# Performance work log

Measured on AMD Instinct MI355X. Metric: run time of the kernel, lower is better.

Reference implementation:

```python
import jax, jax.numpy as jnp
import numpy as np

B, T, INP, E, H, N = 16, 256, 1536, 512, 8, 16
D = E // H            # 64, must equal default dim_head for to_out shapes to work
SCALE = D ** -0.5
EPS = 1e-5


def _ln(x, g, b):
    m = x.mean(-1, keepdims=True)
    v = ((x - m) ** 2).mean(-1, keepdims=True)
    return (x - m) * jax.lax.rsqrt(v + EPS) * g + b


def _attend(q, k, v, Wo, bo):
    # q,k,v: [bt, h, n, d]. NOTE: attend is LogSoftmax, not Softmax (faithful).
    dots = jnp.einsum('bhnd,bhmd->bhnm', q, k) * SCALE
    a = jax.nn.log_softmax(dots, axis=-1)
    o = jnp.einsum('bhnm,bhmd->bhnd', a, v)
    o = o.transpose(0, 2, 1, 3).reshape(o.shape[0], N, E)  # b n (h d)
    return o @ Wo + bo


def _self_attn(x, Wqkv, Wo, bo):
    # x is already LayerNormed (PreNorm); residual adds the normed x (faithful).
    qkv = x @ Wqkv  # [bt, n, 3E]
    q, k, v = jnp.split(qkv, 3, axis=-1)
    hd = lambda t: t.reshape(t.shape[0], N, H, D).transpose(0, 2, 1, 3)
    return _attend(hd(q), hd(k), hd(v), Wo, bo) + x


def _ff(x, W1, b1, W2, b2):
    # x already LayerNormed; residual adds normed x (faithful to PreNorm+FF).
    return jax.nn.gelu(x @ W1 + b1, approximate=False) @ W2 + b2 + x


def setup_inputs() -> dict:
    key = jax.random.key(0)
    ks = iter(jax.random.split(key, 64))
    nrm = lambda shape, s=0.02: jax.random.normal(next(ks), shape, jnp.float32) * s
    inp = {
        'features': jax.random.normal(next(ks), (B, T, INP), jnp.float32),
        'targets_array': jax.random.randint(next(ks), (B, T), 0, N, jnp.int64),
        'emb': nrm((N, E), 1.0),
        'Wf': nrm((INP, 2 * E * N)), 'bf': jnp.zeros((2 * E * N,), jnp.float32),
        # layer 0: Attention (tuple path: only to_out used)
        'att0_Wo': nrm((E, E)), 'att0_bo': jnp.zeros((E,), jnp.float32),
        'Wm': nrm((E, 1)), 'bm': jnp.zeros((1,), jnp.float32),
    }
    for i in range(3):
        inp[f'ff{i}_g'] = jnp.ones((E,), jnp.float32)
        inp[f'ff{i}_b'] = jnp.zeros((E,), jnp.float32)
        inp[f'ff{i}_W1'] = nrm((E, 2 * E)); inp[f'ff{i}_b1'] = jnp.zeros((2 * E,), jnp.float32)
        inp[f'ff{i}_W2'] = nrm((2 * E, E)); inp[f'ff{i}_b2'] = jnp.zeros((E,), jnp.float32)
    for i in (1, 2):
        inp[f'att{i}_g'] = jnp.ones((E,), jnp.float32)
        inp[f'att{i}_b'] = jnp.zeros((E,), jnp.float32)
        inp[f'att{i}_Wqkv'] = nrm((E, 3 * E))
        inp[f'att{i}_Wo'] = nrm((E, E)); inp[f'att{i}_bo'] = jnp.zeros((E,), jnp.float32)
    return inp


def reference(features, targets_array, emb, Wf, bf, att0_Wo, att0_bo, Wm, bm,
              ff0_g, ff0_b, ff0_W1, ff0_b1, ff0_W2, ff0_b2,
              ff1_g, ff1_b, ff1_W1, ff1_b1, ff1_W2, ff1_b2,
              ff2_g, ff2_b, ff2_W1, ff2_b1, ff2_W2, ff2_b2,
              att1_g, att1_b, att1_Wqkv, att1_Wo, att1_bo,
              att2_g, att2_b, att2_Wqkv, att2_Wo, att2_bo):
    f = features.reshape(-1, INP)                 # [BT, INP]
    t = targets_array.reshape(-1)                 # [BT]
    kv = f @ Wf + bf                              # [BT, 2*E*N]
    k_, v_ = jnp.split(kv, 2, axis=-1)
    nhd = lambda x: x.reshape(-1, N, H, D).transpose(0, 2, 1, 3)  # b (n h d) -> b h n d
    k, v = nhd(k_), nhd(v_)
    q = emb[t].reshape(-1, H, 1, D)               # b h d -> b h 1 d
    q = jnp.broadcast_to(q, (q.shape[0], H, N, D))
    # layer stack: Attn(tuple), PreNorm(FF), PreNorm(Attn), PreNorm(FF), PreNorm(Attn), PreNorm(FF)
    x = _attend(q, k, v, att0_Wo, att0_bo)        # [BT, N, E]
    x = _ff(_ln(x, ff0_g, ff0_b), ff0_W1, ff0_b1, ff0_W2, ff0_b2)
    x = _self_attn(_ln(x, att1_g, att1_b), att1_Wqkv, att1_Wo, att1_bo)
    x = _ff(_ln(x, ff1_g, ff1_b), ff1_W1, ff1_b1, ff1_W2, ff1_b2)
    x = _self_attn(_ln(x, att2_g, att2_b), att2_Wqkv, att2_Wo, att2_bo)
    x = _ff(_ln(x, ff2_g, ff2_b), ff2_W1, ff2_b1, ff2_W2, ff2_b2)
    out = x.mean(axis=1)                          # mean over targets -> [BT, E]
    out = out.reshape(B, T, E)
    mean = out @ Wm + bm                          # [B, T, 1]
    return mean
```

## Files before the change

kernel.cpp:

```cpp
#include <hip/hip_runtime.h>
#include <math.h>

#define BTOT 4096
#define INP  1536
#define EDIM 512
#define NTOK 16
#define KVW  16384
#define ENW  8192
#define FFH  1024
#define NDOT 2048

typedef __attribute__((ext_vector_type(8))) __bf16 bf16x8;
typedef __attribute__((ext_vector_type(4))) float f32x4;

__device__ __forceinline__ ushort f2bf(float f) {
    union { float f; unsigned u; } v; v.f = f;
    unsigned r = v.u + 0x7fffu + ((v.u >> 16) & 1u);
    return (ushort)(r >> 16);
}
__device__ __forceinline__ float bf2f(ushort h) {
    union { unsigned u; float f; } v; v.u = ((unsigned)h) << 16;
    return v.f;
}

struct TJob { const float* in; ushort* out; int ld, c0, R, gbx, boffs; };

struct PrepArgs {
    const float* features; ushort* featb;
    const float* wq0; const float* wq1; ushort* wv0; ushort* wv1;
    const float* Wf; const float* bfv; const float* emb;
    ushort* BTg; float* C0s; const int* targets; int* perm; int* boff;
    TJob tj[10];
};

__global__ __launch_bounds__(256) void prep_all_k(PrepArgs A)
{
    __shared__ float t[64][65];
    __shared__ int cnt[NTOK], off_s[NTOK], cur[NTOK];
    const int b = blockIdx.x;
    const int tid = threadIdx.x;

    if (b < 3328) {
        if (b < 3072) {
            const int i = b * 256 + tid;
            const float4* p = reinterpret_cast<const float4*>(A.features) + 2 * (size_t)i;
            float4 a = p[0], c = p[1];
            uint4 o;
            o.x = f2bf(a.x) | ((unsigned)f2bf(a.y) << 16);
            o.y = f2bf(a.z) | ((unsigned)f2bf(a.w) << 16);
            o.z = f2bf(c.x) | ((unsigned)f2bf(c.y) << 16);
            o.w = f2bf(c.z) | ((unsigned)f2bf(c.w) << 16);
            reinterpret_cast<uint4*>(A.featb)[i] = o;
        } else {
            const int bb = b - 3072;
            const float* src = (bb >= 128) ? A.wq1 : A.wq0;
            ushort* dst = (bb >= 128) ? A.wv1 : A.wv0;
            const int idx = (bb & 127) * 256 + tid;
            const int row = idx >> 6, c8 = (idx & 63) * 8;
            const float4* p = reinterpret_cast<const float4*>(
                src + (size_t)row * (3 * EDIM) + 2 * EDIM + c8);
            float4 a = p[0], c = p[1];
            uint4 o;
            o.x = f2bf(a.x) | ((unsigned)f2bf(a.y) << 16);
            o.y = f2bf(a.z) | ((unsigned)f2bf(a.w) << 16);
            o.z = f2bf(c.x) | ((unsigned)f2bf(c.y) << 16);
            o.w = f2bf(c.z) | ((unsigned)f2bf(c.w) << 16);
            *reinterpret_cast<uint4*>(dst + (size_t)row * EDIM + c8) = o;
        }
        return;
    }

    if (b < 4480) {
        const int gb = b - 3328;
        const int hm = gb & 127;
        const int gby = gb >> 7;
        if (gby == 8) {
            if (hm != 0) return;
            if (tid < NTOK) cnt[tid] = 0;
            __syncthreads();
            for (int i = tid; i < BTOT; i += 256) atomicAdd(&cnt[A.targets[i]], 1);
            __syncthreads();
            if (tid == 0) {
                int s = 0;
                for (int bk = 0; bk < NTOK; ++bk) { off_s[bk] = s; cur[bk] = s; s += cnt[bk]; }
                for (int bk = 0; bk < NTOK; ++bk) A.boff[bk] = off_s[bk];
                A.boff[NTOK] = s;
            }
            __syncthreads();
            for (int i = tid; i < BTOT; i += 256) {
                int tt = A.targets[i];
                int p = atomicAdd(&cur[tt], 1);
                A.perm[p] = i;
            }
            return;
        }
        const int h = hm >> 4, m = hm & 15;
        const int l = tid & 63, w = tid >> 6;
        const int tk = l & 15, isub = l >> 4;
        const int colb = m * 512 + h * 64;
        const int ibase = gby * (INP / 8);

        float4 e[16];
#pragma unroll
        for (int q = 0; q < 16; ++q)
            e[q] = *reinterpret_cast<const float4*>(A.emb + tk * EDIM + h * 64 + q * 4);

        const int n = tk * 128 + hm;
        for (int i0 = ibase; i0 < ibase + INP / 8; i0 += 16) {
            const int i = i0 + w * 4 + isub;
            const float* wr = A.Wf + (size_t)i * KVW + colb;
            float acc = 0.f;
#pragma unroll
            for (int q = 0; q < 16; ++q) {
                float4 v4 = *reinterpret_cast<const float4*>(wr + q * 4);
                acc = fmaf(v4.x, e[q].x, fmaf(v4.y, e[q].y,
                      fmaf(v4.z, e[q].z, fmaf(v4.w, e[q].w, acc))));
            }
            A.BTg[(size_t)n * INP + i] = f2bf(acc);
        }
        if (gby == 0 && w == 0 && isub == 0) {
            const float* br = A.bfv + colb;
            float acc = 0.f;
#pragma unroll
            for (int q = 0; q < 16; ++q) {
                float4 v4 = *reinterpret_cast<const float4*>(br + q * 4);
                acc = fmaf(v4.x, e[q].x, fmaf(v4.y, e[q].y,
                      fmaf(v4.z, e[q].z, fmaf(v4.w, e[q].w, acc))));
            }
            A.C0s[n] = 0.125f * acc;
        }
        return;
    }

    const int rel = b - 4480;
    int ji = 0;
    while (ji < 9 && rel >= A.tj[ji + 1].boffs) ++ji;
    TJob jb = A.tj[ji];
    const int r2 = rel - jb.boffs;
    const int bx = r2 % jb.gbx, by = r2 / jb.gbx;

    const int bc = bx * 64 + jb.c0;
    const int br = by * 64;
#pragma unroll
    for (int it = 0; it < 16; ++it) {
        int idx = tid + it * 256;
        int r = idx >> 6, c = idx & 63;
        t[r][c] = jb.in[(size_t)(br + r) * jb.ld + bc + c];
    }
    __syncthreads();
    const int C0 = bx * 64;
#pragma unroll
    for (int it = 0; it < 4; ++it) {
        int idx = tid + it * 256;
        int cc = idx >> 4, rp = idx & 15;
        uint2 w2;
        w2.x = f2bf(t[4 * rp + 0][cc]) | ((unsigned)f2bf(t[4 * rp + 1][cc]) << 16);
        w2.y = f2bf(t[4 * rp + 2][cc]) | ((unsigned)f2bf(t[4 * rp + 3][cc]) << 16);
        *reinterpret_cast<uint2*>(jb.out + (size_t)(C0 + cc) * jb.R + br + 4 * rp) = w2;
    }
}

template <int BM, int BN, int WM, int WN, int NW, bool GELU, bool OUTBF>
__global__ __launch_bounds__(NW * 64) void gemm_mfma_k(
    const ushort* __restrict__ A, int lda,
    const ushort* __restrict__ BT, int ldb,
    void* __restrict__ Cp, int ldc, int K,
    const float* __restrict__ bias,
    const float* __restrict__ res, int ldr,
    float scale)
{
    static_assert((BM / WM) * (BN / WN) == NW, "wave grid");
    static_assert(BM % (NW * 8) == 0 && BN % (NW * 8) == 0, "staging");
    constexpr int FM = WM / 16, FN = WN / 16;
    constexpr int IA = BM * 8 / (NW * 64), IB = BN * 8 / (NW * 64);
    constexpr int RA = BM / NW, RB = BN / NW;

    __shared__ bf16x8 As[BM][8];
    __shared__ bf16x8 Bs[BN][8];
    const int tid = threadIdx.x;
    const int l   = tid & 63;
    const int w   = tid >> 6;
    const int wm  = w / (BN / WN), wn = w % (BN / WN);
    const int brow = blockIdx.y * BM, bcol = blockIdx.x * BN;

    const int lr = l >> 3;
    const int ls = (l & 7) ^ lr;
    const ushort* Ab = A  + (size_t)(brow + w * RA + lr) * lda + ls * 8;
    const ushort* Bb = BT + (size_t)(bcol + w * RB + lr) * ldb + ls * 8;

    f32x4 acc[FM][FN];
#pragma unroll
    for (int i = 0; i < FM; ++i)
#pragma unroll
        for (int j = 0; j < FN; ++j) acc[i][j] = (f32x4)0.f;

    for (int k0 = 0; k0 < K; k0 += 64) {
#pragma unroll
        for (int i = 0; i < IA; ++i)
            __builtin_amdgcn_global_load_lds(
                (const __attribute__((address_space(1))) void*)(Ab + (size_t)(i * 8) * lda + k0),
                (__attribute__((address_space(3))) void*)&As[w * RA + i * 8][0],
                16, 0, 0);
#pragma unroll
        for (int i = 0; i < IB; ++i)
            __builtin_amdgcn_global_load_lds(
                (const __attribute__((address_space(1))) void*)(Bb + (size_t)(i * 8) * ldb + k0),
                (__attribute__((address_space(3))) void*)&Bs[w * RB + i * 8][0],
                16, 0, 0);
        __syncthreads();
#pragma unroll
        for (int kh = 0; kh < 2; ++kh) {
            const int slot = (kh * 4 + (l >> 4)) ^ (l & 7);
            bf16x8 af[FM], bfr[FN];
#pragma unroll
            for (int mt = 0; mt < FM; ++mt)
                af[mt] = As[wm * WM + mt * 16 + (l & 15)][slot];
#pragma unroll
            for (int nt = 0; nt < FN; ++nt)
                bfr[nt] = Bs[wn * WN + nt * 16 + (l & 15)][slot];
#pragma unroll
            for (int mt = 0; mt < FM; ++mt)
#pragma unroll
                for (int nt = 0; nt < FN; ++nt)
                    acc[mt][nt] = __builtin_amdgcn_mfma_f32_16x16x32_bf16(
                        af[mt], bfr[nt], acc[mt][nt], 0, 0, 0);
        }
        __syncthreads();
    }

    const int cr = (l >> 4) * 4, cc = l & 15;
#pragma unroll
    for (int mt = 0; mt < FM; ++mt) {
#pragma unroll
        for (int nt = 0; nt < FN; ++nt) {
            const int gc = bcol + wn * WN + nt * 16 + cc;
            const float bv = bias ? bias[gc] : 0.f;
#pragma unroll
            for (int r = 0; r < 4; ++r) {
                const size_t gr = (size_t)brow + wm * WM + mt * 16 + cr + r;
                float v = acc[mt][nt][r] * scale + bv;
                if (GELU) v = 0.5f * v * (1.f + erff(v * 0.70710678118654752f));
                if (res) v += res[gr * ldr + gc];
                if (OUTBF) ((ushort*)Cp)[gr * ldc + gc] = f2bf(v);
                else       ((float*)Cp)[gr * ldc + gc]  = v;
            }
        }
    }
}

__global__ __launch_bounds__(256) void mega_gemm_k(
    const ushort* __restrict__ featb,
    const ushort* __restrict__ WfvT, const float* __restrict__ bfvv,
    ushort* __restrict__ vb,
    const ushort* __restrict__ BTg,
    const int* __restrict__ perm, const int* __restrict__ boff,
    const float* __restrict__ C0s, float* __restrict__ dsel,
    const ushort* __restrict__ WoT0, const ushort* __restrict__ Wv0,
    ushort* __restrict__ WC0,
    const ushort* __restrict__ WoT1, const ushort* __restrict__ Wv1,
    ushort* __restrict__ WC1)
{
    __shared__ bf16x8 As[128][8];
    __shared__ bf16x8 Bs[128][8];
    const int b = blockIdx.x;
    const int tid = threadIdx.x;
    const int l = tid & 63, w = tid >> 6;
    const int wm = w >> 1, wn = w & 1;
    const int lr = l >> 3, ls = (l & 7) ^ lr;

    int jtype, K;
    const ushort* Asrc[4];
    const ushort* Bb;
    ushort* WCo = nullptr;
    int brow = 0, bcol = 0, bucket = 0, off = 0, end = 0, tile = 0;

    if (b < 2048) {
        jtype = 0; K = INP;
        brow = (b >> 6) * 128; bcol = (b & 63) * 128;
#pragma unroll
        for (int i = 0; i < 4; ++i)
            Asrc[i] = featb + (size_t)(brow + w * 32 + lr + i * 8) * INP + ls * 8;
        Bb = WfvT + (size_t)(bcol + w * 32 + lr) * INP + ls * 8;
    } else if (b < 2560) {
        jtype = 1; K = INP;
        const int rel = b - 2048;
        bucket = rel >> 5; tile = rel & 31;
        off = boff[bucket]; end = boff[bucket + 1];
        if (tile * 128 >= end - off) return;
#pragma unroll
        for (int i = 0; i < 4; ++i) {
            int rg = off + tile * 128 + w * 32 + lr + i * 8;
            Asrc[i] = featb + (size_t)perm[rg < end ? rg : off] * INP + ls * 8;
        }
        Bb = BTg + (size_t)(bucket * 128 + w * 32 + lr) * INP + ls * 8;
    } else {
        jtype = 2; K = EDIM;
        const int rel = b - 2560;
        const int wi = rel >> 4, r2 = rel & 15;
        brow = (r2 >> 2) * 128; bcol = (r2 & 3) * 128;
        const ushort* Ai = wi ? WoT1 : WoT0;
        const ushort* Bi = wi ? Wv1 : Wv0;
        WCo = wi ? WC1 : WC0;
#pragma unroll
        for (int i = 0; i < 4; ++i)
            Asrc[i] = Ai + (size_t)(brow + w * 32 + lr + i * 8) * EDIM + ls * 8;
        Bb = Bi + (size_t)(bcol + w * 32 + lr) * EDIM + ls * 8;
    }

    f32x4 acc[4][4];
#pragma unroll
    for (int i = 0; i < 4; ++i)
#pragma unroll
        for (int j = 0; j < 4; ++j) acc[i][j] = (f32x4)0.f;

    for (int k0 = 0; k0 < K; k0 += 64) {
#pragma unroll
        for (int i = 0; i < 4; ++i)
            __builtin_amdgcn_global_load_lds(
                (const __attribute__((address_space(1))) void*)(Asrc[i] + k0),
                (__attribute__((address_space(3))) void*)&As[w * 32 + i * 8][0],
                16, 0, 0);
#pragma unroll
        for (int i = 0; i < 4; ++i)
            __builtin_amdgcn_global_load_lds(
                (const __attribute__((address_space(1))) void*)(Bb + (size_t)(i * 8) * K + k0),
                (__attribute__((address_space(3))) void*)&Bs[w * 32 + i * 8][0],
                16, 0, 0);
        __syncthreads();
#pragma unroll
        for (int kh = 0; kh < 2; ++kh) {
            const int slot = (kh * 4 + (l >> 4)) ^ (l & 7);
            bf16x8 af[4], bfr[4];
#pragma unroll
            for (int mt = 0; mt < 4; ++mt)
                af[mt] = As[wm * 64 + mt * 16 + (l & 15)][slot];
#pragma unroll
            for (int nt = 0; nt < 4; ++nt)
                bfr[nt] = Bs[wn * 64 + nt * 16 + (l & 15)][slot];
#pragma unroll
            for (int mt = 0; mt < 4; ++mt)
#pragma unroll
                for (int nt = 0; nt < 4; ++nt)
                    acc[mt][nt] = __builtin_amdgcn_mfma_f32_16x16x32_bf16(
                        af[mt], bfr[nt], acc[mt][nt], 0, 0, 0);
        }
        __syncthreads();
    }

    const int cr = (l >> 4) * 4, cc = l & 15;
    const float CATT = -44.36141955583650f;

    if (jtype == 0) {
#pragma unroll
        for (int mt = 0; mt < 4; ++mt) {
#pragma unroll
            for (int nt = 0; nt < 4; ++nt) {
                const int gc = bcol + wn * 64 + nt * 16 + cc;
                const float bv = bfvv[gc];
#pragma unroll
                for (int r = 0; r < 4; ++r) {
                    const size_t gr = (size_t)brow + wm * 64 + mt * 16 + cr + r;
                    vb[gr * ENW + gc] = f2bf(acc[mt][nt][r] + bv);
                }
            }
        }
    } else if (jtype == 1) {
#pragma unroll
        for (int mt = 0; mt < 4; ++mt) {
#pragma unroll
            for (int nt = 0; nt < 4; ++nt) {
                const int gc = wn * 64 + nt * 16 + cc;
                const float bv = C0s[bucket * 128 + gc];
#pragma unroll
                for (int r = 0; r < 4; ++r) {
                    float val = acc[mt][nt][r] * 0.125f + bv;
                    float mx = val;
                    mx = fmaxf(mx, __shfl_xor(mx, 1, 64));
                    mx = fmaxf(mx, __shfl_xor(mx, 2, 64));
                    mx = fmaxf(mx, __shfl_xor(mx, 4, 64));
                    mx = fmaxf(mx, __shfl_xor(mx, 8, 64));
                    float e = expf(val - mx);
                    e += __shfl_xor(e, 1, 64);
                    e += __shfl_xor(e, 2, 64);
                    e += __shfl_xor(e, 4, 64);
                    e += __shfl_xor(e, 8, 64);
                    const float lse = mx + logf(e);
                    int rg = off + tile * 128 + wm * 64 + mt * 16 + cr + r;
                    int orow = perm[rg < end ? rg : off];
                    dsel[(size_t)orow * 128 + gc] = val - lse;
                }
            }
        }
    } else {
#pragma unroll
        for (int mt = 0; mt < 4; ++mt) {
#pragma unroll
            for (int nt = 0; nt < 4; ++nt) {
                const int gc = bcol + wn * 64 + nt * 16 + cc;
#pragma unroll
                for (int r = 0; r < 4; ++r) {
                    const size_t gr = (size_t)brow + wm * 64 + mt * 16 + cr + r;
                    WCo[gr * EDIM + gc] = f2bf(acc[mt][nt][r] * CATT);
                }
            }
        }
    }
}

__global__ __launch_bounds__(512) void attend0_k(
    const float* __restrict__ dsel, const ushort* __restrict__ vb,
    ushort* __restrict__ o)
{
    const int bt = blockIdx.x;
    const int l  = threadIdx.x & 63;
    const int h  = threadIdx.x >> 6;
    const int dg = l & 7, mg = l >> 3;

    const float w0 = dsel[(size_t)bt * 128 + h * 16 + mg];
    const float w1 = dsel[(size_t)bt * 128 + h * 16 + 8 + mg];

    const ushort* base = vb + (size_t)bt * ENW + h * 64 + dg * 8;
    uint4 v0 = *reinterpret_cast<const uint4*>(base + (size_t)mg * EDIM);
    uint4 v1 = *reinterpret_cast<const uint4*>(base + (size_t)(8 + mg) * EDIM);
    const ushort* u0 = reinterpret_cast<const ushort*>(&v0);
    const ushort* u1 = reinterpret_cast<const ushort*>(&v1);
    float acc[8];
#pragma unroll
    for (int j = 0; j < 8; ++j)
        acc[j] = w0 * bf2f(u0[j]) + w1 * bf2f(u1[j]);
#pragma unroll
    for (int off = 8; off < 64; off <<= 1)
#pragma unroll
        for (int j = 0; j < 8; ++j) acc[j] += __shfl_xor(acc[j], off, 64);

    if (mg == 0) {
        uint4 pk;
        pk.x = f2bf(acc[0]) | ((unsigned)f2bf(acc[1]) << 16);
        pk.y = f2bf(acc[2]) | ((unsigned)f2bf(acc[3]) << 16);
        pk.z = f2bf(acc[4]) | ((unsigned)f2bf(acc[5]) << 16);
        pk.w = f2bf(acc[6]) | ((unsigned)f2bf(acc[7]) << 16);
        *reinterpret_cast<uint4*>(o + (size_t)bt * EDIM + h * 64 + dg * 8) = pk;
    }
}

__global__ __launch_bounds__(256) void ln_k(
    const float* __restrict__ x, const float* __restrict__ g,
    const float* __restrict__ b, float* __restrict__ y,
    ushort* __restrict__ yb)
{
    const int row = blockIdx.x * 4 + (threadIdx.x >> 6);
    const int lane = threadIdx.x & 63;
    const float* xr = x + (size_t)row * EDIM + lane * 8;
    float4 a0 = *reinterpret_cast<const float4*>(xr);
    float4 a1 = *reinterpret_cast<const float4*>(xr + 4);
    float v[8] = {a0.x, a0.y, a0.z, a0.w, a1.x, a1.y, a1.z, a1.w};

    float s = 0.f;
#pragma unroll
    for (int j = 0; j < 8; ++j) s += v[j];
#pragma unroll
    for (int off = 32; off; off >>= 1) s += __shfl_xor(s, off, 64);
    const float m = s * (1.f / 512.f);

    float q = 0.f;
#pragma unroll
    for (int j = 0; j < 8; ++j) { float d = v[j] - m; q = fmaf(d, d, q); }
#pragma unroll
    for (int off = 32; off; off >>= 1) q += __shfl_xor(q, off, 64);
    const float inv = rsqrtf(q * (1.f / 512.f) + 1e-5f);

    const int c = lane * 8;
    float4 g0 = *reinterpret_cast<const float4*>(g + c);
    float4 g1 = *reinterpret_cast<const float4*>(g + c + 4);
    float4 b0 = *reinterpret_cast<const float4*>(b + c);
    float4 b1 = *reinterpret_cast<const float4*>(b + c + 4);
    float gg[8] = {g0.x, g0.y, g0.z, g0.w, g1.x, g1.y, g1.z, g1.w};
    float bb[8] = {b0.x, b0.y, b0.z, b0.w, b1.x, b1.y, b1.z, b1.w};
    float out[8];
#pragma unroll
    for (int j = 0; j < 8; ++j) out[j] = (v[j] - m) * inv * gg[j] + bb[j];
    float* yr = y + (size_t)row * EDIM + c;
    *reinterpret_cast<float4*>(yr) = make_float4(out[0], out[1], out[2], out[3]);
    *reinterpret_cast<float4*>(yr + 4) = make_float4(out[4], out[5], out[6], out[7]);
    uint4 p;
    p.x = f2bf(out[0]) | ((unsigned)f2bf(out[1]) << 16);
    p.y = f2bf(out[2]) | ((unsigned)f2bf(out[3]) << 16);
    p.z = f2bf(out[4]) | ((unsigned)f2bf(out[5]) << 16);
    p.w = f2bf(out[6]) | ((unsigned)f2bf(out[7]) << 16);
    *reinterpret_cast<uint4*>(yb + (size_t)row * EDIM + c) = p;
}

__global__ __launch_bounds__(256) void final_k(
    const float* __restrict__ x, const float* __restrict__ Wm,
    const float* __restrict__ bm, float* __restrict__ out)
{
    const int row = blockIdx.x * 4 + (threadIdx.x >> 6);
    const int lane = threadIdx.x & 63;
    const float* xr = x + (size_t)row * EDIM + lane * 8;
    const float* wr = Wm + lane * 8;
    float s = 0.f;
#pragma unroll
    for (int j = 0; j < 8; ++j) s = fmaf(xr[j], wr[j], s);
#pragma unroll
    for (int off = 32; off; off >>= 1) s += __shfl_xor(s, off, 64);
    if (lane == 0) out[row] = s + bm[0];
}

extern "C" void kernel_launch(void* const* d_in, const int* in_sizes, int n_in,
                              void* d_out, int out_size, void* d_ws, size_t ws_size,
                              hipStream_t stream)
{
    (void)in_sizes; (void)n_in; (void)out_size; (void)ws_size;
    const float* features = (const float*)d_in[0];
    const int*   targets  = (const int*)d_in[1];
    const float* emb      = (const float*)d_in[2];
    const float* Wf       = (const float*)d_in[3];
    const float* bfv      = (const float*)d_in[4];
    const float* a0Wo     = (const float*)d_in[5];
    const float* a0bo     = (const float*)d_in[6];
    const float* Wm       = (const float*)d_in[7];
    const float* bm       = (const float*)d_in[8];
    const float *ffg[3], *ffb[3], *W1[3], *b1[3], *W2[3], *b2[3];
    for (int i = 0; i < 3; ++i) {
        ffg[i] = (const float*)d_in[9 + 6 * i];
        ffb[i] = (const float*)d_in[10 + 6 * i];
        W1[i]  = (const float*)d_in[11 + 6 * i];
        b1[i]  = (const float*)d_in[12 + 6 * i];
        W2[i]  = (const float*)d_in[13 + 6 * i];
        b2[i]  = (const float*)d_in[14 + 6 * i];
    }
    const float *ag[2], *abp[2], *aWqkv[2], *aWo[2], *abo[2];
    for (int i = 0; i < 2; ++i) {
        ag[i]    = (const float*)d_in[27 + 5 * i];
        abp[i]   = (const float*)d_in[28 + 5 * i];
        aWqkv[i] = (const float*)d_in[29 + 5 * i];
        aWo[i]   = (const float*)d_in[30 + 5 * i];
        abo[i]   = (const float*)d_in[31 + 5 * i];
    }

    char* wsc = (char*)d_ws;
    auto alloc = [&](size_t bytes) { char* p = wsc; wsc += bytes; return p; };
    ushort* WfvT  = (ushort*)alloc((size_t)ENW * INP * 2);
    ushort* BTg   = (ushort*)alloc((size_t)NDOT * INP * 2);
    float*  C0s   = (float*) alloc((size_t)NDOT * 4);
    float*  dsel  = (float*) alloc((size_t)BTOT * 128 * 4);
    int*    perm  = (int*)   alloc((size_t)BTOT * 4);
    int*    boff  = (int*)   alloc(32 * 4);
    ushort* a0WoT = (ushort*)alloc((size_t)EDIM * EDIM * 2);
    ushort *W1T[3], *W2T[3], *WoT[2], *Wv_bf[2], *WcombT[2];
    for (int i = 0; i < 3; ++i) {
        W1T[i] = (ushort*)alloc((size_t)FFH * EDIM * 2);
        W2T[i] = (ushort*)alloc((size_t)EDIM * FFH * 2);
    }
    for (int i = 0; i < 2; ++i) {
        WoT[i]    = (ushort*)alloc((size_t)EDIM * EDIM * 2);
        Wv_bf[i]  = (ushort*)alloc((size_t)EDIM * EDIM * 2);
        WcombT[i] = (ushort*)alloc((size_t)EDIM * EDIM * 2);
    }
    ushort* featb = (ushort*)alloc((size_t)BTOT * INP * 2);
    ushort* o_b   = (ushort*)alloc((size_t)BTOT * EDIM * 2);
    float*  x     = (float*) alloc((size_t)BTOT * EDIM * 4);
    float*  xln   = (float*) alloc((size_t)BTOT * EDIM * 4);
    ushort* xlnb  = (ushort*)alloc((size_t)BTOT * EDIM * 2);
    ushort* hb    = (ushort*)alloc((size_t)BTOT * FFH * 2);
    ushort* vb    = (ushort*)alloc((size_t)BTOT * ENW * 2);

    const dim3 blk(256, 1, 1);

    PrepArgs pa;
    pa.features = features; pa.featb = featb;
    pa.wq0 = aWqkv[0]; pa.wq1 = aWqkv[1]; pa.wv0 = Wv_bf[0]; pa.wv1 = Wv_bf[1];
    pa.Wf = Wf; pa.bfv = bfv; pa.emb = emb;
    pa.BTg = BTg; pa.C0s = C0s; pa.targets = targets;
    pa.perm = perm; pa.boff = boff;
    int ob = 0, ji = 0;
    auto addj = [&](const float* in, ushort* out, int ld, int c0, int R,
                    int gbx, int gby) {
        pa.tj[ji++] = {in, out, ld, c0, R, gbx, ob};
        ob += gbx * gby;
    };
    addj(Wf, WfvT, KVW, ENW, INP, 128, 24);
    addj(a0Wo, a0WoT, EDIM, 0, EDIM, 8, 8);
    for (int i = 0; i < 3; ++i) {
        addj(W1[i], W1T[i], FFH, 0, EDIM, 16, 8);
        addj(W2[i], W2T[i], EDIM, 0, FFH, 8, 16);
    }
    addj(aWo[0], WoT[0], EDIM, 0, EDIM, 8, 8);
    addj(aWo[1], WoT[1], EDIM, 0, EDIM, 8, 8);
    prep_all_k<<<4480 + ob, blk, 0, stream>>>(pa);

    mega_gemm_k<<<2592, blk, 0, stream>>>(
        featb, WfvT, bfv + ENW, vb,
        BTg, perm, boff, C0s, dsel,
        WoT[0], Wv_bf[0], WcombT[0],
        WoT[1], Wv_bf[1], WcombT[1]);

    attend0_k<<<BTOT, 512, 0, stream>>>(dsel, vb, o_b);
    gemm_mfma_k<64, 128, 32, 64, 4, false, false>
        <<<dim3(EDIM / 128, BTOT / 64), blk, 0, stream>>>(
        o_b, EDIM, a0WoT, EDIM, x, EDIM, EDIM, a0bo, nullptr, 0, 1.f);

    auto ln = [&](const float* g, const float* b) {
        ln_k<<<BTOT / 4, blk, 0, stream>>>(x, g, b, xln, xlnb);
    };
    auto ff = [&](int i) {
        ln(ffg[i], ffb[i]);
        gemm_mfma_k<64, 128, 32, 64, 4, true, true>
            <<<dim3(FFH / 128, BTOT / 64), blk, 0, stream>>>(
            xlnb, EDIM, W1T[i], EDIM, hb, FFH, EDIM, b1[i], nullptr, 0, 1.f);
        gemm_mfma_k<64, 128, 32, 64, 4, false, false>
            <<<dim3(EDIM / 128, BTOT / 64), blk, 0, stream>>>(
            hb, FFH, W2T[i], FFH, x, EDIM, FFH, b2[i], xln, EDIM, 1.f);
    };
    auto attn = [&](int i) {
        ln(ag[i], abp[i]);
        gemm_mfma_k<64, 128, 32, 64, 4, false, false>
            <<<dim3(EDIM / 128, BTOT / 64), blk, 0, stream>>>(
            xlnb, EDIM, WcombT[i], EDIM, x, EDIM, EDIM, abo[i], xln, EDIM, 1.f);
    };

    ff(0);
    attn(0);
    ff(1);
    attn(1);
    ff(2);

    final_k<<<BTOT / 4, blk, 0, stream>>>(x, Wm, bm, (float*)d_out);
}
```

Baseline: 493.5 us.

## Split mega GEMM and give the value projection a 256x256 double-buffered kernel

```diff
diff --git a/kernel.cpp b/kernel.cpp
--- a/kernel.cpp
+++ b/kernel.cpp
@@ -248,64 +248,145 @@
     }
 }
 
-__global__ __launch_bounds__(256) void mega_gemm_k(
-    const ushort* __restrict__ featb,
-    const ushort* __restrict__ WfvT, const float* __restrict__ bfvv,
-    ushort* __restrict__ vb,
-    const ushort* __restrict__ BTg,
+__global__ __launch_bounds__(512, 2) void gemm_v256_k(
+    const ushort* __restrict__ A,
+    const ushort* __restrict__ BT,
+    const float* __restrict__ bias,
+    ushort* __restrict__ C)
+{
+    __shared__ bf16x8 lds[2][2][256][8];
+    const int tid = threadIdx.x;
+    const int l = tid & 63, w = tid >> 6;
+    const int wm = w >> 2, wn = w & 3;
+    const int brow = blockIdx.y * 256, bcol = blockIdx.x * 256;
+    const int lr = l >> 3, ls = (l & 7) ^ lr;
+
+    const ushort* Ab = A  + (size_t)(brow + w * 8 + lr) * INP + ls * 8;
+    const ushort* Bb = BT + (size_t)(bcol + w * 8 + lr) * INP + ls * 8;
+
+#define STAGE_T(d, t) do { const int k0s = (t) * 64;                          \
+    _Pragma("unroll")                                                          \
+    for (int g = 0; g < 4; ++g)                                                \
+        __builtin_amdgcn_global_load_lds(                                      \
+            (const __attribute__((address_space(1))) void*)(Ab + (size_t)(g * 64) * INP + k0s), \
+            (__attribute__((address_space(3))) void*)&lds[d][0][g * 64 + w * 8][0], 16, 0, 0);  \
+    _Pragma("unroll")                                                          \
+    for (int g = 0; g < 4; ++g)                                                \
+        __builtin_amdgcn_global_load_lds(                                      \
+            (const __attribute__((address_space(1))) void*)(Bb + (size_t)(g * 64) * INP + k0s), \
+            (__attribute__((address_space(3))) void*)&lds[d][1][g * 64 + w * 8][0], 16, 0, 0);  \
+} while (0)
+
+    f32x4 acc[8][4];
+#pragma unroll
+    for (int i = 0; i < 8; ++i)
+#pragma unroll
+        for (int j = 0; j < 4; ++j) acc[i][j] = (f32x4)0.f;
+
+    STAGE_T(0, 0);
+    STAGE_T(1, 1);
+    asm volatile("s_waitcnt vmcnt(8)" ::: "memory");
+    __builtin_amdgcn_s_barrier();
+
+    const int NT = INP / 64;
+    for (int j = 0; j < NT; ++j) {
+        const int d = j & 1;
+        if (j > 0 && j < NT - 1) STAGE_T(d ^ 1, j + 1);
+        bf16x8 a0[4][2], bfr[4][2];
+#pragma unroll
+        for (int mt = 0; mt < 4; ++mt)
+#pragma unroll
+            for (int kh = 0; kh < 2; ++kh)
+                a0[mt][kh] = lds[d][0][wm * 128 + mt * 16 + (l & 15)]
+                                [(kh * 4 + (l >> 4)) ^ (l & 7)];
+#pragma unroll
+        for (int nt = 0; nt < 4; ++nt)
+#pragma unroll
+            for (int kh = 0; kh < 2; ++kh)
+                bfr[nt][kh] = lds[d][1][wn * 64 + nt * 16 + (l & 15)]
+                                 [(kh * 4 + (l >> 4)) ^ (l & 7)];
+        __builtin_amdgcn_s_barrier();
+        asm volatile("s_waitcnt lgkmcnt(0)" ::: "memory");
+        __builtin_amdgcn_sched_barrier(0);
+        __builtin_amdgcn_s_setprio(1);
+#pragma unroll
+        for (int mt = 0; mt < 4; ++mt)
+#pragma unroll
+            for (int nt = 0; nt < 4; ++nt)
+#pragma unroll
+                for (int kh = 0; kh < 2; ++kh)
+                    acc[mt][nt] = __builtin_amdgcn_mfma_f32_16x16x32_bf16(
+                        a0[mt][kh], bfr[nt][kh], acc[mt][nt], 0, 0, 0);
+        __builtin_amdgcn_s_setprio(0);
+        __builtin_amdgcn_s_barrier();
+        bf16x8 a1[4][2];
+#pragma unroll
+        for (int mt = 0; mt < 4; ++mt)
+#pragma unroll
+            for (int kh = 0; kh < 2; ++kh)
+                a1[mt][kh] = lds[d][0][wm * 128 + 64 + mt * 16 + (l & 15)]
+                                [(kh * 4 + (l >> 4)) ^ (l & 7)];
+        __builtin_amdgcn_s_barrier();
+        asm volatile("s_waitcnt lgkmcnt(0)" ::: "memory");
+        __builtin_amdgcn_sched_barrier(0);
+        __builtin_amdgcn_s_setprio(1);
+#pragma unroll
+        for (int mt = 0; mt < 4; ++mt)
+#pragma unroll
+            for (int nt = 0; nt < 4; ++nt)
+#pragma unroll
+                for (int kh = 0; kh < 2; ++kh)
+                    acc[4 + mt][nt] = __builtin_amdgcn_mfma_f32_16x16x32_bf16(
+                        a1[mt][kh], bfr[nt][kh], acc[4 + mt][nt], 0, 0, 0);
+        __builtin_amdgcn_s_setprio(0);
+        asm volatile("s_waitcnt vmcnt(0)" ::: "memory");
+        __builtin_amdgcn_s_barrier();
+    }
+#undef STAGE_T
+
+    const int cr = (l >> 4) * 4, cc = l & 15;
+#pragma unroll
+    for (int h = 0; h < 2; ++h)
+#pragma unroll
+        for (int mt = 0; mt < 4; ++mt)
+#pragma unroll
+            for (int nt = 0; nt < 4; ++nt) {
+                const int gc = bcol + wn * 64 + nt * 16 + cc;
+                const float bv = bias[gc];
+#pragma unroll
+                for (int r = 0; r < 4; ++r) {
+                    const size_t gr = (size_t)brow + wm * 128 + h * 64 + mt * 16 + cr + r;
+                    C[gr * ENW + gc] = f2bf(acc[h * 4 + mt][nt][r] + bv);
+                }
+            }
+}
+
+__global__ __launch_bounds__(256) void gemm_dots_k(
+    const ushort* __restrict__ A,
+    const ushort* __restrict__ BT,
     const int* __restrict__ perm, const int* __restrict__ boff,
-    const float* __restrict__ C0s, float* __restrict__ dsel,
-    const ushort* __restrict__ WoT0, const ushort* __restrict__ Wv0,
-    ushort* __restrict__ WC0,
-    const ushort* __restrict__ WoT1, const ushort* __restrict__ Wv1,
-    ushort* __restrict__ WC1)
-{
+    const float* __restrict__ C0s, float* __restrict__ Csel)
+{
+    const int bucket = blockIdx.y;
+    const int off = boff[bucket], end = boff[bucket + 1];
+    const int tile = blockIdx.x;
+    if (tile * 128 >= end - off) return;
+
     __shared__ bf16x8 As[128][8];
     __shared__ bf16x8 Bs[128][8];
-    const int b = blockIdx.x;
     const int tid = threadIdx.x;
     const int l = tid & 63, w = tid >> 6;
     const int wm = w >> 1, wn = w & 1;
-    const int lr = l >> 3, ls = (l & 7) ^ lr;
-
-    int jtype, K;
-    const ushort* Asrc[4];
-    const ushort* Bb;
-    ushort* WCo = nullptr;
-    int brow = 0, bcol = 0, bucket = 0, off = 0, end = 0, tile = 0;
-
-    if (b < 2048) {
-        jtype = 0; K = INP;
-        brow = (b >> 6) * 128; bcol = (b & 63) * 128;
-#pragma unroll
-        for (int i = 0; i < 4; ++i)
-            Asrc[i] = featb + (size_t)(brow + w * 32 + lr + i * 8) * INP + ls * 8;
-        Bb = WfvT + (size_t)(bcol + w * 32 + lr) * INP + ls * 8;
-    } else if (b < 2560) {
-        jtype = 1; K = INP;
-        const int rel = b - 2048;
-        bucket = rel >> 5; tile = rel & 31;
-        off = boff[bucket]; end = boff[bucket + 1];
-        if (tile * 128 >= end - off) return;
-#pragma unroll
-        for (int i = 0; i < 4; ++i) {
-            int rg = off + tile * 128 + w * 32 + lr + i * 8;
-            Asrc[i] = featb + (size_t)perm[rg < end ? rg : off] * INP + ls * 8;
-        }
-        Bb = BTg + (size_t)(bucket * 128 + w * 32 + lr) * INP + ls * 8;
-    } else {
-        jtype = 2; K = EDIM;
-        const int rel = b - 2560;
-        const int wi = rel >> 4, r2 = rel & 15;
-        brow = (r2 >> 2) * 128; bcol = (r2 & 3) * 128;
-        const ushort* Ai = wi ? WoT1 : WoT0;
-        const ushort* Bi = wi ? Wv1 : Wv0;
-        WCo = wi ? WC1 : WC0;
-#pragma unroll
-        for (int i = 0; i < 4; ++i)
-            Asrc[i] = Ai + (size_t)(brow + w * 32 + lr + i * 8) * EDIM + ls * 8;
-        Bb = Bi + (size_t)(bcol + w * 32 + lr) * EDIM + ls * 8;
-    }
+    const int lr = l >> 3;
+    const int ls = (l & 7) ^ lr;
+
+    int rowidx[4];
+#pragma unroll
+    for (int i = 0; i < 4; ++i) {
+        int rg = off + tile * 128 + w * 32 + lr + i * 8;
+        rowidx[i] = perm[rg < end ? rg : off];
+    }
+    const ushort* Bb = BT + (size_t)(bucket * 128 + w * 32 + lr) * INP + ls * 8;
 
     f32x4 acc[4][4];
 #pragma unroll
@@ -313,17 +394,19 @@
 #pragma unroll
         for (int j = 0; j < 4; ++j) acc[i][j] = (f32x4)0.f;
 
-    for (int k0 = 0; k0 < K; k0 += 64) {
+    for (int k0 = 0; k0 < INP; k0 += 64) {
 #pragma unroll
         for (int i = 0; i < 4; ++i)
             __builtin_amdgcn_global_load_lds(
-                (const __attribute__((address_space(1))) void*)(Asrc[i] + k0),
+                (const __attribute__((address_space(1))) void*)(
+                    A + (size_t)rowidx[i] * INP + ls * 8 + k0),
                 (__attribute__((address_space(3))) void*)&As[w * 32 + i * 8][0],
                 16, 0, 0);
 #pragma unroll
         for (int i = 0; i < 4; ++i)
             __builtin_amdgcn_global_load_lds(
-                (const __attribute__((address_space(1))) void*)(Bb + (size_t)(i * 8) * K + k0),
+                (const __attribute__((address_space(1))) void*)(
+                    Bb + (size_t)(i * 8) * INP + k0),
                 (__attribute__((address_space(3))) void*)&Bs[w * 32 + i * 8][0],
                 16, 0, 0);
         __syncthreads();
@@ -348,60 +431,29 @@
     }
 
     const int cr = (l >> 4) * 4, cc = l & 15;
-    const float CATT = -44.36141955583650f;
-
-    if (jtype == 0) {
-#pragma unroll
-        for (int mt = 0; mt < 4; ++mt) {
-#pragma unroll
-            for (int nt = 0; nt < 4; ++nt) {
-                const int gc = bcol + wn * 64 + nt * 16 + cc;
-                const float bv = bfvv[gc];
-#pragma unroll
-                for (int r = 0; r < 4; ++r) {
-                    const size_t gr = (size_t)brow + wm * 64 + mt * 16 + cr + r;
-                    vb[gr * ENW + gc] = f2bf(acc[mt][nt][r] + bv);
-                }
-            }
-        }
-    } else if (jtype == 1) {
-#pragma unroll
-        for (int mt = 0; mt < 4; ++mt) {
-#pragma unroll
-            for (int nt = 0; nt < 4; ++nt) {
-                const int gc = wn * 64 + nt * 16 + cc;
-                const float bv = C0s[bucket * 128 + gc];
-#pragma unroll
-                for (int r = 0; r < 4; ++r) {
-                    float val = acc[mt][nt][r] * 0.125f + bv;
-                    float mx = val;
-                    mx = fmaxf(mx, __shfl_xor(mx, 1, 64));
-                    mx = fmaxf(mx, __shfl_xor(mx, 2, 64));
-                    mx = fmaxf(mx, __shfl_xor(mx, 4, 64));
-                    mx = fmaxf(mx, __shfl_xor(mx, 8, 64));
-                    float e = expf(val - mx);
-                    e += __shfl_xor(e, 1, 64);
-                    e += __shfl_xor(e, 2, 64);
-                    e += __shfl_xor(e, 4, 64);
-                    e += __shfl_xor(e, 8, 64);
-                    const float lse = mx + logf(e);
-                    int rg = off + tile * 128 + wm * 64 + mt * 16 + cr + r;
-                    int orow = perm[rg < end ? rg : off];
-                    dsel[(size_t)orow * 128 + gc] = val - lse;
-                }
-            }
-        }
-    } else {
-#pragma unroll
-        for (int mt = 0; mt < 4; ++mt) {
-#pragma unroll
-            for (int nt = 0; nt < 4; ++nt) {
-                const int gc = bcol + wn * 64 + nt * 16 + cc;
-#pragma unroll
-                for (int r = 0; r < 4; ++r) {
-                    const size_t gr = (size_t)brow + wm * 64 + mt * 16 + cr + r;
-                    WCo[gr * EDIM + gc] = f2bf(acc[mt][nt][r] * CATT);
-                }
+#pragma unroll
+    for (int mt = 0; mt < 4; ++mt) {
+#pragma unroll
+        for (int nt = 0; nt < 4; ++nt) {
+            const int gc = wn * 64 + nt * 16 + cc;
+            const float bv = C0s[bucket * 128 + gc];
+#pragma unroll
+            for (int r = 0; r < 4; ++r) {
+                float val = acc[mt][nt][r] * 0.125f + bv;
+                float mx = val;
+                mx = fmaxf(mx, __shfl_xor(mx, 1, 64));
+                mx = fmaxf(mx, __shfl_xor(mx, 2, 64));
+                mx = fmaxf(mx, __shfl_xor(mx, 4, 64));
+                mx = fmaxf(mx, __shfl_xor(mx, 8, 64));
+                float e = expf(val - mx);
+                e += __shfl_xor(e, 1, 64);
+                e += __shfl_xor(e, 2, 64);
+                e += __shfl_xor(e, 4, 64);
+                e += __shfl_xor(e, 8, 64);
+                const float lse = mx + logf(e);
+                int rg = off + tile * 128 + wm * 64 + mt * 16 + cr + r;
+                int orow = perm[rg < end ? rg : off];
+                Csel[(size_t)orow * 128 + gc] = val - lse;
             }
         }
     }
@@ -589,12 +641,16 @@
     addj(aWo[1], WoT[1], EDIM, 0, EDIM, 8, 8);
     prep_all_k<<<4480 + ob, blk, 0, stream>>>(pa);
 
-    mega_gemm_k<<<2592, blk, 0, stream>>>(
-        featb, WfvT, bfv + ENW, vb,
-        BTg, perm, boff, C0s, dsel,
-        WoT[0], Wv_bf[0], WcombT[0],
-        WoT[1], Wv_bf[1], WcombT[1]);
-
+    const float CATT = -44.36141955583650f;
+    gemm_dots_k<<<dim3(32, 16), blk, 0, stream>>>(featb, BTg, perm, boff,
+                                                  C0s, dsel);
+    for (int i = 0; i < 2; ++i)
+        gemm_mfma_k<64, 128, 32, 64, 4, false, true>
+            <<<dim3(EDIM / 128, EDIM / 64), blk, 0, stream>>>(
+            WoT[i], EDIM, Wv_bf[i], EDIM, WcombT[i], EDIM, EDIM,
+            nullptr, nullptr, 0, CATT);
+    gemm_v256_k<<<dim3(ENW / 256, BTOT / 256), dim3(512, 1, 1), 0, stream>>>(
+        featb, WfvT, bfv + ENW, vb);
     attend0_k<<<BTOT, 512, 0, stream>>>(dsel, vb, o_b);
     gemm_mfma_k<64, 128, 32, 64, 4, false, false>
         <<<dim3(EDIM / 128, BTOT / 64), blk, 0, stream>>>(
```

Result: no change. 498.4 us (+1.0%).
